# Performance work log

Measured on AMD Instinct MI355X. Metric: run time of the kernel, lower is better.

The kernel has to match this reference:

```python
import jax, jax.numpy as jnp
import numpy as np

N = 8192        # points
M = 131072      # query-key pairs (edges)
C_IN = 512
H = 8           # heads
D = 64          # head_channels
BINS = 48
BIN_SIZE = 0.05


def setup_inputs() -> dict:
    key = jax.random.key(0)
    ks = jax.random.split(key, 8)
    x_F = jax.random.normal(ks[0], (N, C_IN), dtype=jnp.float32)
    x_C = jax.random.uniform(ks[1], (N, 3), dtype=jnp.float32)
    qk_pair_idxs = jax.random.randint(ks[2], (2, M), 0, N, dtype=jnp.int64)
    W_qkv = jax.random.normal(ks[3], (C_IN, 3 * H * D), dtype=jnp.float32) * 0.02
    b_qkv = jnp.zeros((3 * H * D,), dtype=jnp.float32)
    q_tables = jax.random.normal(ks[4], (3, BINS, H, D), dtype=jnp.float32) * 0.02
    k_tables = jax.random.normal(ks[5], (3, BINS, H, D), dtype=jnp.float32) * 0.02
    v_tables = jax.random.normal(ks[6], (3, BINS, H, D), dtype=jnp.float32) * 0.02
    return {"x_F": x_F, "x_C": x_C, "qk_pair_idxs": qk_pair_idxs,
            "W_qkv": W_qkv, "b_qkv": b_qkv,
            "q_tables": q_tables, "k_tables": k_tables, "v_tables": v_tables}


def reference(x_F, x_C, qk_pair_idxs, W_qkv, b_qkv, q_tables, k_tables, v_tables):
    n = x_F.shape[0]
    qkv = (x_F @ W_qkv + b_qkv).reshape(n, 3, H, D)
    q = qkv[:, 0] * (D ** -0.5)   # scale folded into queries, as in the module
    k = qkv[:, 1]
    v = qkv[:, 2]
    qi = qk_pair_idxs[0]
    ki = qk_pair_idxs[1]
    # quantized relative coordinates -> table bin indices [M,3]
    rel = (x_C[qi] - x_C[ki]) / BIN_SIZE + BINS / 2
    idx = jnp.clip(rel.astype(jnp.int32), 0, BINS - 1)
    # precompute per-point, per-axis, per-bin table dot products [N,3,BINS,H]
    q_dot = jnp.einsum('nhd,abhd->nabh', q, q_tables)
    k_dot = jnp.einsum('nhd,abhd->nabh', k, k_tables)
    # content logits [M,H]
    logits = jnp.einsum('mhd,mhd->mh', q[qi], k[ki])
    for a in range(3):  # fixed xyz axes
        logits = logits + q_dot[qi, a, idx[:, a]] + k_dot[ki, a, idx[:, a]]
    # scatter softmax over query index (per head)
    seg_max = jax.ops.segment_max(logits, qi, num_segments=n)
    e = jnp.exp(logits - seg_max[qi])
    denom = jax.ops.segment_sum(e, qi, num_segments=n)
    attn = e / denom[qi]  # [M,H]
    # value-side relative position bias, summed over axes [M,H,D]
    vt = v_tables[0, idx[:, 0]] + v_tables[1, idx[:, 1]] + v_tables[2, idx[:, 2]]
    contrib = attn[:, :, None] * (v[ki] + vt)            # [M,H,D]
    agg = jax.ops.segment_sum(contrib, qi, num_segments=n)  # [N,H,D]
    return agg.reshape(n, H * D)
```

## Files before the change

kernel.cpp:

```cpp
#include <hip/hip_runtime.h>
#include <hip/hip_bf16.h>
#include <stdint.h>

#define N_PTS 8192
#define M_EDGES 131072
#define CIN 512
#define QKV_COLS 1536

typedef __bf16 bf16x8 __attribute__((ext_vector_type(8)));
typedef float f32x4 __attribute__((ext_vector_type(4)));

#define GAS __attribute__((address_space(1)))
#define LAS __attribute__((address_space(3)))

__device__ __forceinline__ void gload_lds16(const void* g, void* l) {
  __builtin_amdgcn_global_load_lds((const GAS void*)g, (LAS void*)l, 16, 0, 0);
}

__global__ void cast_a(const float* __restrict__ x, __bf16* __restrict__ a) {
  int i = blockIdx.x * blockDim.x + threadIdx.x;
  int base = i * 4;
  if (base < N_PTS * CIN) {
    float4 v = *(const float4*)(x + base);
    a[base + 0] = (__bf16)v.x;
    a[base + 1] = (__bf16)v.y;
    a[base + 2] = (__bf16)v.z;
    a[base + 3] = (__bf16)v.w;
  }
}

__global__ void cast_bt(const float* __restrict__ w, __bf16* __restrict__ bt) {
  __shared__ float tile[32][33];
  int bk = blockIdx.x, bn = blockIdx.y;
  int x = threadIdx.x & 31, y = threadIdx.x >> 5;
#pragma unroll
  for (int j = 0; j < 4; j++) {
    int r = y + j * 8;
    tile[r][x] = w[(size_t)(bk * 32 + r) * QKV_COLS + bn * 32 + x];
  }
  __syncthreads();
#pragma unroll
  for (int j = 0; j < 4; j++) {
    int r = y + j * 8;
    bt[(size_t)(bn * 32 + r) * CIN + bk * 32 + x] = (__bf16)tile[x][r];
  }
}

__global__ void cast_tables(const float* __restrict__ qt, const float* __restrict__ kt,
                            const float* __restrict__ vt, __bf16* __restrict__ qtb,
                            __bf16* __restrict__ ktb, __bf16* __restrict__ vtb) {
  int i = blockIdx.x * 256 + threadIdx.x;
  if (i >= 3 * 48 * 512) return;
  int d = i & 63, h = (i >> 6) & 7, ab = i >> 9;
  int po = (h * 144 + ab) * 64 + d;
  qtb[po] = (__bf16)qt[i];
  ktb[po] = (__bf16)kt[i];
  vtb[i] = (__bf16)vt[i];
}

__global__ __launch_bounds__(256) void gemm_qkv(const __bf16* __restrict__ A,
                                                const __bf16* __restrict__ BT,
                                                const float* __restrict__ bias,
                                                __bf16* __restrict__ qb,
                                                __bf16* __restrict__ kb,
                                                __bf16* __restrict__ vb) {
  __shared__ __align__(16) char At[128 * 32 * 2];
  __shared__ __align__(16) char Bt[128 * 32 * 2];
  int tid = threadIdx.x;
  int w = tid >> 6, l = tid & 63;
  int bm = blockIdx.x, bn = blockIdx.y;
  int wm = w & 1, wn = w >> 1;
  f32x4 acc[4][4] = {};
  const char* Ab = (const char*)A;
  const char* Bb = (const char*)BT;

  for (int kt = 0; kt < 16; kt++) {
#pragma unroll
    for (int r = 0; r < 2; r++) {
      int flat = r * 4096 + w * 1024 + l * 16;
      int row = flat >> 6, colb = flat & 63;
      gload_lds16(Ab + ((size_t)(bm * 128 + row) * CIN + kt * 32) * 2 + colb,
                  At + r * 4096 + w * 1024);
      gload_lds16(Bb + ((size_t)(bn * 128 + row) * CIN + kt * 32) * 2 + colb,
                  Bt + r * 4096 + w * 1024);
    }
    __syncthreads();
    bf16x8 af[4], bfr[4];
    int lr = l & 15;
    int lk = (l >> 4) * 16;
#pragma unroll
    for (int mf = 0; mf < 4; mf++) af[mf] = *(const bf16x8*)(At + (wm * 64 + mf * 16 + lr) * 64 + lk);
#pragma unroll
    for (int nf = 0; nf < 4; nf++) bfr[nf] = *(const bf16x8*)(Bt + (wn * 64 + nf * 16 + lr) * 64 + lk);
#pragma unroll
    for (int mf = 0; mf < 4; mf++)
#pragma unroll
      for (int nf = 0; nf < 4; nf++)
        acc[mf][nf] = __builtin_amdgcn_mfma_f32_16x16x32_bf16(af[mf], bfr[nf], acc[mf][nf], 0, 0, 0);
    __syncthreads();
  }

  int lr = l & 15, lg = l >> 4;
#pragma unroll
  for (int mf = 0; mf < 4; mf++) {
#pragma unroll
    for (int nf = 0; nf < 4; nf++) {
      int gc = bn * 128 + wn * 64 + nf * 16 + lr;
      float b = bias[gc];
      int which = gc >> 9;
      int col = gc & 511;
      __bf16* dst = which == 0 ? qb : (which == 1 ? kb : vb);
      float scale = which == 0 ? 0.125f : 1.0f;
#pragma unroll
      for (int j = 0; j < 4; j++) {
        int gr = bm * 128 + wm * 64 + mf * 16 + lg * 4 + j;
        dst[(size_t)gr * 512 + col] = (__bf16)((acc[mf][nf][j] + b) * scale);
      }
    }
  }
}

__global__ __launch_bounds__(256) void table_dot(const __bf16* __restrict__ src,
                                                 const __bf16* __restrict__ tab,
                                                 __bf16* __restrict__ out) {
  __shared__ __align__(16) char As[128 * 128];
  __shared__ __align__(16) char Bs[144 * 128];
  int nt = blockIdx.x, h = blockIdx.y;
  int tid = threadIdx.x, w = tid >> 6, l = tid & 63;
  const char* sb = (const char*)src;
  const char* tb = (const char*)tab + (size_t)h * 144 * 128;
#pragma unroll
  for (int p = 0; p < 4; p++) {
    int flat = p * 4096 + w * 1024 + l * 16;
    int row = flat >> 7, colb = flat & 127;
    gload_lds16(sb + (size_t)(nt * 128 + row) * 1024 + h * 128 + colb, As + p * 4096 + w * 1024);
    gload_lds16(tb + flat, Bs + p * 4096 + w * 1024);
  }
  if (w < 2) {
    int flat = 16384 + w * 1024 + l * 16;
    gload_lds16(tb + flat, Bs + 16384 + w * 1024);
  }
  __syncthreads();

  f32x4 acc[2][9] = {};
  int lr = l & 15, lk = (l >> 4) * 16;
#pragma unroll
  for (int ks = 0; ks < 2; ks++) {
    bf16x8 af[2], bf[9];
#pragma unroll
    for (int mf = 0; mf < 2; mf++)
      af[mf] = *(const bf16x8*)(As + (w * 32 + mf * 16 + lr) * 128 + ks * 64 + lk);
#pragma unroll
    for (int nf = 0; nf < 9; nf++)
      bf[nf] = *(const bf16x8*)(Bs + (nf * 16 + lr) * 128 + ks * 64 + lk);
#pragma unroll
    for (int mf = 0; mf < 2; mf++)
#pragma unroll
      for (int nf = 0; nf < 9; nf++)
        acc[mf][nf] = __builtin_amdgcn_mfma_f32_16x16x32_bf16(af[mf], bf[nf], acc[mf][nf], 0, 0, 0);
  }

  int lg = l >> 4;
#pragma unroll
  for (int mf = 0; mf < 2; mf++)
#pragma unroll
    for (int nf = 0; nf < 9; nf++)
#pragma unroll
      for (int j = 0; j < 4; j++) {
        int n = nt * 128 + w * 32 + mf * 16 + lg * 4 + j;
        int ab = nf * 16 + lr;
        out[(size_t)n * 1152 + ab * 8 + h] = (__bf16)acc[mf][nf][j];
      }
}

__global__ void edge_setup(const int* __restrict__ pairs, const float* __restrict__ xc,
                           int* __restrict__ qi_a, int* __restrict__ ki_a,
                           unsigned* __restrict__ bins, int* __restrict__ cnt) {
  int m = blockIdx.x * blockDim.x + threadIdx.x;
  if (m >= M_EDGES) return;
  int qi = pairs[m], ki = pairs[M_EDGES + m];
  unsigned pb = 0;
#pragma unroll
  for (int a = 0; a < 3; a++) {
    float rel = (xc[qi * 3 + a] - xc[ki * 3 + a]) / 0.05f + 24.0f;
    int b = (int)rel;
    b = b < 0 ? 0 : (b > 47 ? 47 : b);
    pb |= (unsigned)b << (6 * a);
  }
  qi_a[m] = qi;
  ki_a[m] = ki;
  bins[m] = pb;
  atomicAdd(&cnt[qi], 1);
}

__global__ __launch_bounds__(256) void scan_kernel(const int* __restrict__ cnt,
                                                   int* __restrict__ off,
                                                   int* __restrict__ cursor) {
  __shared__ int wsum[4];
  int tid = threadIdx.x, lane = tid & 63, w = tid >> 6;
  int local[32];
  int s = 0;
#pragma unroll
  for (int i = 0; i < 8; i++) {
    int4 v = ((const int4*)cnt)[tid * 8 + i];
    local[i * 4 + 0] = v.x; local[i * 4 + 1] = v.y;
    local[i * 4 + 2] = v.z; local[i * 4 + 3] = v.w;
    s += v.x + v.y + v.z + v.w;
  }
  int incl = s;
#pragma unroll
  for (int d = 1; d < 64; d <<= 1) {
    int t = __shfl_up(incl, d, 64);
    if (lane >= d) incl += t;
  }
  if (lane == 63) wsum[w] = incl;
  __syncthreads();
  int woff = 0;
#pragma unroll
  for (int j = 0; j < 4; j++) woff += (j < w) ? wsum[j] : 0;
  int run = woff + incl - s;
  int base = tid * 32;
#pragma unroll
  for (int i = 0; i < 32; i++) {
    off[base + i] = run;
    cursor[base + i] = run;
    run += local[i];
  }
  if (tid == 255) off[N_PTS] = run;
}

__global__ void scatter_k(const int* __restrict__ qi_a, const int* __restrict__ ki_a,
                          const unsigned* __restrict__ bins, int* __restrict__ cursor,
                          int* __restrict__ qi_s, int* __restrict__ ki_s,
                          unsigned* __restrict__ bins_s) {
  int m = blockIdx.x * blockDim.x + threadIdx.x;
  if (m < M_EDGES) {
    int qi = qi_a[m];
    int pos = atomicAdd(&cursor[qi], 1);
    qi_s[pos] = qi;
    ki_s[pos] = ki_a[m];
    bins_s[pos] = bins[m];
  }
}

__global__ void edge_bias(const int* __restrict__ qi_s, const int* __restrict__ ki_s,
                          const unsigned* __restrict__ bins_s, const __bf16* __restrict__ qdot,
                          const __bf16* __restrict__ kdot, float* __restrict__ eb) {
  int t = blockIdx.x * 256 + threadIdx.x;
  int e = t >> 3, h = t & 7;
  if (e >= M_EDGES) return;
  int qi = qi_s[e], ki = ki_s[e];
  unsigned pb = bins_s[e];
  int a0 = ((int)(pb & 63)) * 8 + h;
  int a1 = (48 + (int)((pb >> 6) & 63)) * 8 + h;
  int a2 = (96 + (int)((pb >> 12) & 63)) * 8 + h;
  const __bf16* qd = qdot + (size_t)qi * 1152;
  const __bf16* kd = kdot + (size_t)ki * 1152;
  eb[t] = (float)qd[a0] + (float)qd[a1] + (float)qd[a2] +
          (float)kd[a0] + (float)kd[a1] + (float)kd[a2];
}

__global__ __launch_bounds__(512) void attn_kernel(
    const __bf16* __restrict__ qb, const __bf16* __restrict__ kb,
    const __bf16* __restrict__ vb, const __bf16* __restrict__ vtb,
    const float* __restrict__ eb, const int* __restrict__ off,
    const int* __restrict__ ki_s, const unsigned* __restrict__ bins_s,
    float* __restrict__ out) {
  int n = blockIdx.x;
  int tid = threadIdx.x;
  int h = tid >> 6, l = tid & 63;
  int es = l >> 3;
  int dg = l & 7;
  int tcol = h * 64 + dg * 8;

  bf16x8 q8 = *(const bf16x8*)(qb + (size_t)n * 512 + tcol);
  float qv[8];
#pragma unroll
  for (int j = 0; j < 8; j++) qv[j] = (float)q8[j];

  float acc[8] = {0.f, 0.f, 0.f, 0.f, 0.f, 0.f, 0.f, 0.f};
  float den = 0.f;
  int e0 = off[n], e1 = off[n + 1];

  for (int base = e0; base < e1; base += 8) {
    int e = base + es;
    bool valid = e < e1;
    int ee = valid ? e : e0;
    int ki = ki_s[ee];
    unsigned pb = bins_s[ee];
    float ebv = eb[(size_t)ee * 8 + h];
    bf16x8 k8 = *(const bf16x8*)(kb + (size_t)ki * 512 + tcol);
    bf16x8 v8 = *(const bf16x8*)(vb + (size_t)ki * 512 + tcol);
    int b0 = pb & 63, b1 = (pb >> 6) & 63, b2 = (pb >> 12) & 63;
    bf16x8 t0 = *(const bf16x8*)(vtb + (size_t)b0 * 512 + tcol);
    bf16x8 t1 = *(const bf16x8*)(vtb + (size_t)(48 + b1) * 512 + tcol);
    bf16x8 t2 = *(const bf16x8*)(vtb + (size_t)(96 + b2) * 512 + tcol);
    float p = 0.f;
#pragma unroll
    for (int j = 0; j < 8; j++) p += qv[j] * (float)k8[j];
    p += __shfl_xor(p, 1, 64);
    p += __shfl_xor(p, 2, 64);
    p += __shfl_xor(p, 4, 64);
    p += ebv;
    float ex = valid ? __expf(p) : 0.f;
    den += ex;
#pragma unroll
    for (int j = 0; j < 8; j++)
      acc[j] += ex * ((float)v8[j] + (float)t0[j] + (float)t1[j] + (float)t2[j]);
  }

#pragma unroll
  for (int s = 8; s <= 32; s <<= 1) {
    den += __shfl_xor(den, s, 64);
#pragma unroll
    for (int j = 0; j < 8; j++) acc[j] += __shfl_xor(acc[j], s, 64);
  }

  if (l < 8) {
    float inv = (e1 > e0) ? 1.f / den : 0.f;
    float* op = out + (size_t)n * 512 + h * 64 + l * 8;
    f32x4 o0 = {acc[0] * inv, acc[1] * inv, acc[2] * inv, acc[3] * inv};
    f32x4 o1 = {acc[4] * inv, acc[5] * inv, acc[6] * inv, acc[7] * inv};
    *(f32x4*)op = o0;
    *(f32x4*)(op + 4) = o1;
  }
}

extern "C" void kernel_launch(void* const* d_in, const int* in_sizes, int n_in,
                              void* d_out, int out_size, void* d_ws, size_t ws_size,
                              hipStream_t stream) {
  const float* xF = (const float*)d_in[0];
  const float* xC = (const float*)d_in[1];
  const int* pairs = (const int*)d_in[2];
  const float* W = (const float*)d_in[3];
  const float* bias = (const float*)d_in[4];
  const float* qt = (const float*)d_in[5];
  const float* kt = (const float*)d_in[6];
  const float* vt = (const float*)d_in[7];
  float* out = (float*)d_out;

  char* ws = (char*)d_ws;
  size_t o = 0;
  auto alloc = [&](size_t bytes) {
    void* p = ws + o;
    o = (o + bytes + 255) & ~(size_t)255;
    return p;
  };
  __bf16* A = (__bf16*)alloc((size_t)N_PTS * CIN * 2);
  __bf16* BT = (__bf16*)alloc((size_t)QKV_COLS * CIN * 2);
  __bf16* qb = (__bf16*)alloc((size_t)N_PTS * 512 * 2);
  __bf16* kb = (__bf16*)alloc((size_t)N_PTS * 512 * 2);
  __bf16* vb = (__bf16*)alloc((size_t)N_PTS * 512 * 2);
  __bf16* qtb = (__bf16*)alloc((size_t)8 * 144 * 64 * 2);
  __bf16* ktb = (__bf16*)alloc((size_t)8 * 144 * 64 * 2);
  __bf16* vtb = (__bf16*)alloc((size_t)144 * 512 * 2);
  __bf16* qdot = (__bf16*)alloc((size_t)N_PTS * 1152 * 2);
  __bf16* kdot = (__bf16*)alloc((size_t)N_PTS * 1152 * 2);
  float* eb = (float*)alloc((size_t)M_EDGES * 8 * 4);
  int* qi_a = (int*)alloc(M_EDGES * 4);
  int* ki_a = (int*)alloc(M_EDGES * 4);
  unsigned* bins = (unsigned*)alloc(M_EDGES * 4);
  int* qi_s = (int*)alloc(M_EDGES * 4);
  int* ki_s = (int*)alloc(M_EDGES * 4);
  unsigned* bins_s = (unsigned*)alloc(M_EDGES * 4);
  int* cnt = (int*)alloc(N_PTS * 4);
  int* off = (int*)alloc((N_PTS + 1) * 4);
  int* cursor = (int*)alloc(N_PTS * 4);

  hipMemsetAsync(cnt, 0, N_PTS * 4, stream);

  cast_a<<<(N_PTS * CIN / 4 + 255) / 256, 256, 0, stream>>>(xF, A);
  cast_bt<<<dim3(CIN / 32, QKV_COLS / 32), 256, 0, stream>>>(W, BT);
  cast_tables<<<(3 * 48 * 512 + 255) / 256, 256, 0, stream>>>(qt, kt, vt, qtb, ktb, vtb);
  gemm_qkv<<<dim3(N_PTS / 128, QKV_COLS / 128), 256, 0, stream>>>(A, BT, bias, qb, kb, vb);
  table_dot<<<dim3(N_PTS / 128, 8), 256, 0, stream>>>(qb, qtb, qdot);
  table_dot<<<dim3(N_PTS / 128, 8), 256, 0, stream>>>(kb, ktb, kdot);
  edge_setup<<<M_EDGES / 256, 256, 0, stream>>>(pairs, xC, qi_a, ki_a, bins, cnt);
  scan_kernel<<<1, 256, 0, stream>>>(cnt, off, cursor);
  scatter_k<<<M_EDGES / 256, 256, 0, stream>>>(qi_a, ki_a, bins, cursor, qi_s, ki_s, bins_s);
  edge_bias<<<(M_EDGES * 8) / 256, 256, 0, stream>>>(qi_s, ki_s, bins_s, qdot, kdot, eb);
  attn_kernel<<<N_PTS, 512, 0, stream>>>(qb, kb, vb, vtb, eb, off, ki_s, bins_s, out);
}
```

Before: 172.0 us.

## Fuse prep kernels, swizzle LDS tiles, pack edge data, unroll attention loop

Merges the cast kernels and edge setup into one launch, and merges the two table_dot launches into one grid with a z dimension. The GEMM now uses a 64-wide K tile with XOR-swizzled LDS layout, and table_dot uses the same swizzle, both to reduce bank conflicts and barrier count. Key index and bins are packed into one 32-bit word to cut index traffic. The attention loop processes two edge groups per iteration to expose more memory-level parallelism, at the cost of more registers.

```diff
diff --git a/kernel.cpp b/kernel.cpp
--- a/kernel.cpp
+++ b/kernel.cpp
@@ -17,45 +17,61 @@
   __builtin_amdgcn_global_load_lds((const GAS void*)g, (LAS void*)l, 16, 0, 0);
 }
 
-__global__ void cast_a(const float* __restrict__ x, __bf16* __restrict__ a) {
-  int i = blockIdx.x * blockDim.x + threadIdx.x;
-  int base = i * 4;
-  if (base < N_PTS * CIN) {
-    float4 v = *(const float4*)(x + base);
-    a[base + 0] = (__bf16)v.x;
-    a[base + 1] = (__bf16)v.y;
-    a[base + 2] = (__bf16)v.z;
-    a[base + 3] = (__bf16)v.w;
-  }
-}
-
-__global__ void cast_bt(const float* __restrict__ w, __bf16* __restrict__ bt) {
+__global__ __launch_bounds__(256) void prep_kernel(
+    const float* __restrict__ xF, const float* __restrict__ W,
+    const float* __restrict__ qt, const float* __restrict__ kt,
+    const float* __restrict__ vt, const int* __restrict__ pairs,
+    const float* __restrict__ xc,
+    __bf16* __restrict__ A, __bf16* __restrict__ BT,
+    __bf16* __restrict__ qtb, __bf16* __restrict__ ktb, __bf16* __restrict__ vtb,
+    int* __restrict__ qi_a, unsigned* __restrict__ pack0, int* __restrict__ cnt) {
   __shared__ float tile[32][33];
-  int bk = blockIdx.x, bn = blockIdx.y;
-  int x = threadIdx.x & 31, y = threadIdx.x >> 5;
-#pragma unroll
-  for (int j = 0; j < 4; j++) {
-    int r = y + j * 8;
-    tile[r][x] = w[(size_t)(bk * 32 + r) * QKV_COLS + bn * 32 + x];
-  }
-  __syncthreads();
-#pragma unroll
-  for (int j = 0; j < 4; j++) {
-    int r = y + j * 8;
-    bt[(size_t)(bn * 32 + r) * CIN + bk * 32 + x] = (__bf16)tile[x][r];
-  }
-}
-
-__global__ void cast_tables(const float* __restrict__ qt, const float* __restrict__ kt,
-                            const float* __restrict__ vt, __bf16* __restrict__ qtb,
-                            __bf16* __restrict__ ktb, __bf16* __restrict__ vtb) {
-  int i = blockIdx.x * 256 + threadIdx.x;
-  if (i >= 3 * 48 * 512) return;
-  int d = i & 63, h = (i >> 6) & 7, ab = i >> 9;
-  int po = (h * 144 + ab) * 64 + d;
-  qtb[po] = (__bf16)qt[i];
-  ktb[po] = (__bf16)kt[i];
-  vtb[i] = (__bf16)vt[i];
+  int b = blockIdx.x;
+  int tid = threadIdx.x;
+  if (b < 4096) {
+    int base = (b * 256 + tid) * 4;
+    float4 v = *(const float4*)(xF + base);
+    A[base + 0] = (__bf16)v.x;
+    A[base + 1] = (__bf16)v.y;
+    A[base + 2] = (__bf16)v.z;
+    A[base + 3] = (__bf16)v.w;
+  } else if (b < 4864) {
+    int blk = b - 4096;
+    int bk = blk & 15, bn = blk >> 4;
+    int x = tid & 31, y = tid >> 5;
+#pragma unroll
+    for (int j = 0; j < 4; j++) {
+      int r = y + j * 8;
+      tile[r][x] = W[(size_t)(bk * 32 + r) * QKV_COLS + bn * 32 + x];
+    }
+    __syncthreads();
+#pragma unroll
+    for (int j = 0; j < 4; j++) {
+      int r = y + j * 8;
+      BT[(size_t)(bn * 32 + r) * CIN + bk * 32 + x] = (__bf16)tile[x][r];
+    }
+  } else if (b < 5152) {
+    int i = (b - 4864) * 256 + tid;
+    int d = i & 63, h = (i >> 6) & 7, ab = i >> 9;
+    int po = (h * 144 + ab) * 64 + d;
+    qtb[po] = (__bf16)qt[i];
+    ktb[po] = (__bf16)kt[i];
+    vtb[i] = (__bf16)vt[i];
+  } else {
+    int m = (b - 5152) * 256 + tid;
+    int qi = pairs[m], ki = pairs[M_EDGES + m];
+    unsigned pb = 0;
+#pragma unroll
+    for (int a = 0; a < 3; a++) {
+      float rel = (xc[qi * 3 + a] - xc[ki * 3 + a]) / 0.05f + 24.0f;
+      int bb = (int)rel;
+      bb = bb < 0 ? 0 : (bb > 47 ? 47 : bb);
+      pb |= (unsigned)bb << (6 * a);
+    }
+    qi_a[m] = qi;
+    pack0[m] = (unsigned)ki | (pb << 13);
+    atomicAdd(&cnt[qi], 1);
+  }
 }
 
 __global__ __launch_bounds__(256) void gemm_qkv(const __bf16* __restrict__ A,
@@ -64,8 +80,8 @@
                                                 __bf16* __restrict__ qb,
                                                 __bf16* __restrict__ kb,
                                                 __bf16* __restrict__ vb) {
-  __shared__ __align__(16) char At[128 * 32 * 2];
-  __shared__ __align__(16) char Bt[128 * 32 * 2];
+  __shared__ __align__(16) char At[128 * 128];
+  __shared__ __align__(16) char Bt[128 * 128];
   int tid = threadIdx.x;
   int w = tid >> 6, l = tid & 63;
   int bm = blockIdx.x, bn = blockIdx.y;
@@ -73,34 +89,40 @@
   f32x4 acc[4][4] = {};
   const char* Ab = (const char*)A;
   const char* Bb = (const char*)BT;
-
-  for (int kt = 0; kt < 16; kt++) {
-#pragma unroll
-    for (int r = 0; r < 2; r++) {
-      int flat = r * 4096 + w * 1024 + l * 16;
-      int row = flat >> 6, colb = flat & 63;
-      gload_lds16(Ab + ((size_t)(bm * 128 + row) * CIN + kt * 32) * 2 + colb,
+  int lr = l & 15;
+  int lk = (l >> 4) * 16;
+  int xr = (lr & 7) << 4;
+
+  for (int kt = 0; kt < 8; kt++) {
+#pragma unroll
+    for (int r = 0; r < 4; r++) {
+      int flat = r * 4096 + tid * 16;
+      int row = flat >> 7, colb = flat & 127;
+      int gcolb = colb ^ ((row & 7) << 4);
+      gload_lds16(Ab + ((size_t)(bm * 128 + row) * CIN + kt * 64) * 2 + gcolb,
                   At + r * 4096 + w * 1024);
-      gload_lds16(Bb + ((size_t)(bn * 128 + row) * CIN + kt * 32) * 2 + colb,
+      gload_lds16(Bb + ((size_t)(bn * 128 + row) * CIN + kt * 64) * 2 + gcolb,
                   Bt + r * 4096 + w * 1024);
     }
     __syncthreads();
-    bf16x8 af[4], bfr[4];
-    int lr = l & 15;
-    int lk = (l >> 4) * 16;
-#pragma unroll
-    for (int mf = 0; mf < 4; mf++) af[mf] = *(const bf16x8*)(At + (wm * 64 + mf * 16 + lr) * 64 + lk);
-#pragma unroll
-    for (int nf = 0; nf < 4; nf++) bfr[nf] = *(const bf16x8*)(Bt + (wn * 64 + nf * 16 + lr) * 64 + lk);
-#pragma unroll
-    for (int mf = 0; mf < 4; mf++)
-#pragma unroll
-      for (int nf = 0; nf < 4; nf++)
-        acc[mf][nf] = __builtin_amdgcn_mfma_f32_16x16x32_bf16(af[mf], bfr[nf], acc[mf][nf], 0, 0, 0);
+#pragma unroll
+    for (int ks = 0; ks < 2; ks++) {
+      bf16x8 af[4], bfr[4];
+      int cs = (ks * 64 + lk) ^ xr;
+#pragma unroll
+      for (int mf = 0; mf < 4; mf++) af[mf] = *(const bf16x8*)(At + (wm * 64 + mf * 16 + lr) * 128 + cs);
+#pragma unroll
+      for (int nf = 0; nf < 4; nf++) bfr[nf] = *(const bf16x8*)(Bt + (wn * 64 + nf * 16 + lr) * 128 + cs);
+#pragma unroll
+      for (int mf = 0; mf < 4; mf++)
+#pragma unroll
+        for (int nf = 0; nf < 4; nf++)
+          acc[mf][nf] = __builtin_amdgcn_mfma_f32_16x16x32_bf16(af[mf], bfr[nf], acc[mf][nf], 0, 0, 0);
+    }
     __syncthreads();
   }
 
-  int lr = l & 15, lg = l >> 4;
+  int lg = l >> 4;
 #pragma unroll
   for (int mf = 0; mf < 4; mf++) {
 #pragma unroll
@@ -120,39 +142,50 @@
   }
 }
 
-__global__ __launch_bounds__(256) void table_dot(const __bf16* __restrict__ src,
-                                                 const __bf16* __restrict__ tab,
-                                                 __bf16* __restrict__ out) {
+__global__ __launch_bounds__(256) void table_dot(const __bf16* __restrict__ qb,
+                                                 const __bf16* __restrict__ kb,
+                                                 const __bf16* __restrict__ qtb,
+                                                 const __bf16* __restrict__ ktb,
+                                                 __bf16* __restrict__ qdot,
+                                                 __bf16* __restrict__ kdot) {
   __shared__ __align__(16) char As[128 * 128];
   __shared__ __align__(16) char Bs[144 * 128];
-  int nt = blockIdx.x, h = blockIdx.y;
+  int nt = blockIdx.x, h = blockIdx.y, z = blockIdx.z;
+  const __bf16* src = z ? kb : qb;
+  const __bf16* tab = z ? ktb : qtb;
+  __bf16* out = z ? kdot : qdot;
   int tid = threadIdx.x, w = tid >> 6, l = tid & 63;
   const char* sb = (const char*)src;
   const char* tb = (const char*)tab + (size_t)h * 144 * 128;
 #pragma unroll
   for (int p = 0; p < 4; p++) {
-    int flat = p * 4096 + w * 1024 + l * 16;
+    int flat = p * 4096 + tid * 16;
     int row = flat >> 7, colb = flat & 127;
-    gload_lds16(sb + (size_t)(nt * 128 + row) * 1024 + h * 128 + colb, As + p * 4096 + w * 1024);
-    gload_lds16(tb + flat, Bs + p * 4096 + w * 1024);
+    int gcolb = colb ^ ((row & 7) << 4);
+    gload_lds16(sb + (size_t)(nt * 128 + row) * 1024 + h * 128 + gcolb, As + p * 4096 + w * 1024);
+    gload_lds16(tb + row * 128 + gcolb, Bs + p * 4096 + w * 1024);
   }
   if (w < 2) {
     int flat = 16384 + w * 1024 + l * 16;
-    gload_lds16(tb + flat, Bs + 16384 + w * 1024);
+    int row = flat >> 7, colb = flat & 127;
+    int gcolb = colb ^ ((row & 7) << 4);
+    gload_lds16(tb + row * 128 + gcolb, Bs + 16384 + w * 1024);
   }
   __syncthreads();
 
   f32x4 acc[2][9] = {};
   int lr = l & 15, lk = (l >> 4) * 16;
+  int xr = (lr & 7) << 4;
 #pragma unroll
   for (int ks = 0; ks < 2; ks++) {
     bf16x8 af[2], bf[9];
+    int cs = (ks * 64 + lk) ^ xr;
 #pragma unroll
     for (int mf = 0; mf < 2; mf++)
-      af[mf] = *(const bf16x8*)(As + (w * 32 + mf * 16 + lr) * 128 + ks * 64 + lk);
+      af[mf] = *(const bf16x8*)(As + (w * 32 + mf * 16 + lr) * 128 + cs);
 #pragma unroll
     for (int nf = 0; nf < 9; nf++)
-      bf[nf] = *(const bf16x8*)(Bs + (nf * 16 + lr) * 128 + ks * 64 + lk);
+      bf[nf] = *(const bf16x8*)(Bs + (nf * 16 + lr) * 128 + cs);
 #pragma unroll
     for (int mf = 0; mf < 2; mf++)
 #pragma unroll
@@ -171,26 +204,6 @@
         int ab = nf * 16 + lr;
         out[(size_t)n * 1152 + ab * 8 + h] = (__bf16)acc[mf][nf][j];
       }
-}
-
-__global__ void edge_setup(const int* __restrict__ pairs, const float* __restrict__ xc,
-                           int* __restrict__ qi_a, int* __restrict__ ki_a,
-                           unsigned* __restrict__ bins, int* __restrict__ cnt) {
-  int m = blockIdx.x * blockDim.x + threadIdx.x;
-  if (m >= M_EDGES) return;
-  int qi = pairs[m], ki = pairs[M_EDGES + m];
-  unsigned pb = 0;
-#pragma unroll
-  for (int a = 0; a < 3; a++) {
-    float rel = (xc[qi * 3 + a] - xc[ki * 3 + a]) / 0.05f + 24.0f;
-    int b = (int)rel;
-    b = b < 0 ? 0 : (b > 47 ? 47 : b);
-    pb |= (unsigned)b << (6 * a);
-  }
-  qi_a[m] = qi;
-  ki_a[m] = ki;
-  bins[m] = pb;
-  atomicAdd(&cnt[qi], 1);
 }
 
 __global__ __launch_bounds__(256) void scan_kernel(const int* __restrict__ cnt,
@@ -229,33 +242,32 @@
   if (tid == 255) off[N_PTS] = run;
 }
 
-__global__ void scatter_k(const int* __restrict__ qi_a, const int* __restrict__ ki_a,
-                          const unsigned* __restrict__ bins, int* __restrict__ cursor,
-                          int* __restrict__ qi_s, int* __restrict__ ki_s,
-                          unsigned* __restrict__ bins_s) {
+__global__ void scatter_k(const int* __restrict__ qi_a, const unsigned* __restrict__ pack0,
+                          int* __restrict__ cursor, int* __restrict__ qi_s,
+                          unsigned* __restrict__ epack) {
   int m = blockIdx.x * blockDim.x + threadIdx.x;
   if (m < M_EDGES) {
     int qi = qi_a[m];
     int pos = atomicAdd(&cursor[qi], 1);
     qi_s[pos] = qi;
-    ki_s[pos] = ki_a[m];
-    bins_s[pos] = bins[m];
-  }
-}
-
-__global__ void edge_bias(const int* __restrict__ qi_s, const int* __restrict__ ki_s,
-                          const unsigned* __restrict__ bins_s, const __bf16* __restrict__ qdot,
-                          const __bf16* __restrict__ kdot, float* __restrict__ eb) {
+    epack[pos] = pack0[m];
+  }
+}
+
+__global__ void edge_bias(const int* __restrict__ qi_s, const unsigned* __restrict__ epack,
+                          const __bf16* __restrict__ qdot, const __bf16* __restrict__ kdot,
+                          float* __restrict__ eb) {
   int t = blockIdx.x * 256 + threadIdx.x;
   int e = t >> 3, h = t & 7;
-  if (e >= M_EDGES) return;
-  int qi = qi_s[e], ki = ki_s[e];
-  unsigned pb = bins_s[e];
+  unsigned pk = epack[e];
+  int ki = pk & 8191;
+  unsigned pb = pk >> 13;
+  int qi = qi_s[e];
   int a0 = ((int)(pb & 63)) * 8 + h;
   int a1 = (48 + (int)((pb >> 6) & 63)) * 8 + h;
   int a2 = (96 + (int)((pb >> 12) & 63)) * 8 + h;
-  const __bf16* qd = qdot + (size_t)qi * 1152;
-  const __bf16* kd = kdot + (size_t)ki * 1152;
+  const __bf16* qd = qdot + qi * 1152;
+  const __bf16* kd = kdot + ki * 1152;
   eb[t] = (float)qd[a0] + (float)qd[a1] + (float)qd[a2] +
           (float)kd[a0] + (float)kd[a1] + (float)kd[a2];
 }
@@ -264,16 +276,14 @@
     const __bf16* __restrict__ qb, const __bf16* __restrict__ kb,
     const __bf16* __restrict__ vb, const __bf16* __restrict__ vtb,
     const float* __restrict__ eb, const int* __restrict__ off,
-    const int* __restrict__ ki_s, const unsigned* __restrict__ bins_s,
-    float* __restrict__ out) {
+    const unsigned* __restrict__ epack, float* __restrict__ out) {
   int n = blockIdx.x;
   int tid = threadIdx.x;
   int h = tid >> 6, l = tid & 63;
-  int es = l >> 3;
-  int dg = l & 7;
+  int es = l >> 3, dg = l & 7;
   int tcol = h * 64 + dg * 8;
 
-  bf16x8 q8 = *(const bf16x8*)(qb + (size_t)n * 512 + tcol);
+  bf16x8 q8 = *(const bf16x8*)(qb + (n << 9) + tcol);
   float qv[8];
 #pragma unroll
   for (int j = 0; j < 8; j++) qv[j] = (float)q8[j];
@@ -282,31 +292,46 @@
   float den = 0.f;
   int e0 = off[n], e1 = off[n + 1];
 
-  for (int base = e0; base < e1; base += 8) {
-    int e = base + es;
-    bool valid = e < e1;
-    int ee = valid ? e : e0;
-    int ki = ki_s[ee];
-    unsigned pb = bins_s[ee];
-    float ebv = eb[(size_t)ee * 8 + h];
-    bf16x8 k8 = *(const bf16x8*)(kb + (size_t)ki * 512 + tcol);
-    bf16x8 v8 = *(const bf16x8*)(vb + (size_t)ki * 512 + tcol);
-    int b0 = pb & 63, b1 = (pb >> 6) & 63, b2 = (pb >> 12) & 63;
-    bf16x8 t0 = *(const bf16x8*)(vtb + (size_t)b0 * 512 + tcol);
-    bf16x8 t1 = *(const bf16x8*)(vtb + (size_t)(48 + b1) * 512 + tcol);
-    bf16x8 t2 = *(const bf16x8*)(vtb + (size_t)(96 + b2) * 512 + tcol);
-    float p = 0.f;
-#pragma unroll
-    for (int j = 0; j < 8; j++) p += qv[j] * (float)k8[j];
-    p += __shfl_xor(p, 1, 64);
-    p += __shfl_xor(p, 2, 64);
-    p += __shfl_xor(p, 4, 64);
-    p += ebv;
-    float ex = valid ? __expf(p) : 0.f;
-    den += ex;
+  for (int base = e0; base < e1; base += 16) {
+    int eA = base + es;
+    int eB = base + 8 + es;
+    int cA = eA < e1 ? eA : e1 - 1;
+    int cB = eB < e1 ? eB : e1 - 1;
+    unsigned pA = epack[cA], pB = epack[cB];
+    float ebA = eb[(cA << 3) + h], ebB = eb[(cB << 3) + h];
+    int kiA = pA & 8191, kiB = pB & 8191;
+    unsigned bA = pA >> 13, bB = pB >> 13;
+    bf16x8 kA8 = *(const bf16x8*)(kb + (kiA << 9) + tcol);
+    bf16x8 vA8 = *(const bf16x8*)(vb + (kiA << 9) + tcol);
+    bf16x8 kB8 = *(const bf16x8*)(kb + (kiB << 9) + tcol);
+    bf16x8 vB8 = *(const bf16x8*)(vb + (kiB << 9) + tcol);
+    bf16x8 tA0 = *(const bf16x8*)(vtb + ((bA & 63u) << 9) + tcol);
+    bf16x8 tA1 = *(const bf16x8*)(vtb + ((48 + ((bA >> 6) & 63u)) << 9) + tcol);
+    bf16x8 tA2 = *(const bf16x8*)(vtb + ((96 + ((bA >> 12) & 63u)) << 9) + tcol);
+    bf16x8 tB0 = *(const bf16x8*)(vtb + ((bB & 63u) << 9) + tcol);
+    bf16x8 tB1 = *(const bf16x8*)(vtb + ((48 + ((bB >> 6) & 63u)) << 9) + tcol);
+    bf16x8 tB2 = *(const bf16x8*)(vtb + ((96 + ((bB >> 12) & 63u)) << 9) + tcol);
+    float p1 = 0.f, p2 = 0.f;
+#pragma unroll
+    for (int j = 0; j < 8; j++) {
+      p1 += qv[j] * (float)kA8[j];
+      p2 += qv[j] * (float)kB8[j];
+    }
+    p1 += __shfl_xor(p1, 1, 64);
+    p2 += __shfl_xor(p2, 1, 64);
+    p1 += __shfl_xor(p1, 2, 64);
+    p2 += __shfl_xor(p2, 2, 64);
+    p1 += __shfl_xor(p1, 4, 64);
+    p2 += __shfl_xor(p2, 4, 64);
+    p1 += ebA;
+    p2 += ebB;
+    float x1 = (eA < e1) ? __expf(p1) : 0.f;
+    float x2 = (eB < e1) ? __expf(p2) : 0.f;
+    den += x1 + x2;
 #pragma unroll
     for (int j = 0; j < 8; j++)
-      acc[j] += ex * ((float)v8[j] + (float)t0[j] + (float)t1[j] + (float)t2[j]);
+      acc[j] += x1 * ((float)vA8[j] + (float)tA0[j] + (float)tA1[j] + (float)tA2[j]) +
+                x2 * ((float)vB8[j] + (float)tB0[j] + (float)tB1[j] + (float)tB2[j]);
   }
 
 #pragma unroll
@@ -318,7 +343,7 @@
 
   if (l < 8) {
     float inv = (e1 > e0) ? 1.f / den : 0.f;
-    float* op = out + (size_t)n * 512 + h * 64 + l * 8;
+    float* op = out + (n << 9) + h * 64 + l * 8;
     f32x4 o0 = {acc[0] * inv, acc[1] * inv, acc[2] * inv, acc[3] * inv};
     f32x4 o1 = {acc[4] * inv, acc[5] * inv, acc[6] * inv, acc[7] * inv};
     *(f32x4*)op = o0;
@@ -358,26 +383,21 @@
   __bf16* kdot = (__bf16*)alloc((size_t)N_PTS * 1152 * 2);
   float* eb = (float*)alloc((size_t)M_EDGES * 8 * 4);
   int* qi_a = (int*)alloc(M_EDGES * 4);
-  int* ki_a = (int*)alloc(M_EDGES * 4);
-  unsigned* bins = (unsigned*)alloc(M_EDGES * 4);
+  unsigned* pack0 = (unsigned*)alloc(M_EDGES * 4);
   int* qi_s = (int*)alloc(M_EDGES * 4);
-  int* ki_s = (int*)alloc(M_EDGES * 4);
-  unsigned* bins_s = (unsigned*)alloc(M_EDGES * 4);
+  unsigned* epack = (unsigned*)alloc(M_EDGES * 4);
   int* cnt = (int*)alloc(N_PTS * 4);
   int* off = (int*)alloc((N_PTS + 1) * 4);
   int* cursor = (int*)alloc(N_PTS * 4);
 
   hipMemsetAsync(cnt, 0, N_PTS * 4, stream);
 
-  cast_a<<<(N_PTS * CIN / 4 + 255) / 256, 256, 0, stream>>>(xF, A);
-  cast_bt<<<dim3(CIN / 32, QKV_COLS / 32), 256, 0, stream>>>(W, BT);
-  cast_tables<<<(3 * 48 * 512 + 255) / 256, 256, 0, stream>>>(qt, kt, vt, qtb, ktb, vtb);
+  prep_kernel<<<5664, 256, 0, stream>>>(xF, W, qt, kt, vt, pairs, xC,
+                                        A, BT, qtb, ktb, vtb, qi_a, pack0, cnt);
+  scan_kernel<<<1, 256, 0, stream>>>(cnt, off, cursor);
+  scatter_k<<<M_EDGES / 256, 256, 0, stream>>>(qi_a, pack0, cursor, qi_s, epack);
   gemm_qkv<<<dim3(N_PTS / 128, QKV_COLS / 128), 256, 0, stream>>>(A, BT, bias, qb, kb, vb);
-  table_dot<<<dim3(N_PTS / 128, 8), 256, 0, stream>>>(qb, qtb, qdot);
-  table_dot<<<dim3(N_PTS / 128, 8), 256, 0, stream>>>(kb, ktb, kdot);
-  edge_setup<<<M_EDGES / 256, 256, 0, stream>>>(pairs, xC, qi_a, ki_a, bins, cnt);
-  scan_kernel<<<1, 256, 0, stream>>>(cnt, off, cursor);
-  scatter_k<<<M_EDGES / 256, 256, 0, stream>>>(qi_a, ki_a, bins, cursor, qi_s, ki_s, bins_s);
-  edge_bias<<<(M_EDGES * 8) / 256, 256, 0, stream>>>(qi_s, ki_s, bins_s, qdot, kdot, eb);
-  attn_kernel<<<N_PTS, 512, 0, stream>>>(qb, kb, vb, vtb, eb, off, ki_s, bins_s, out);
-}
+  table_dot<<<dim3(N_PTS / 128, 8, 2), 256, 0, stream>>>(qb, kb, qtb, ktb, qdot, kdot);
+  edge_bias<<<(M_EDGES * 8) / 256, 256, 0, stream>>>(qi_s, epack, qdot, kdot, eb);
+  attn_kernel<<<N_PTS, 512, 0, stream>>>(qb, kb, vb, vtb, eb, off, epack, out);
+}
```

Result: no change. 169.5 us (-1.4%).
